# Kernel tuning notes

Hardware: AMD Instinct MI355X
Metric: run time of the kernel (lower is better)

## Reference

```python
import jax, jax.numpy as jnp
import numpy as np

EMBED_DIM = 1024
NUM_HEADS = 16
HEAD_DIM = EMBED_DIM // NUM_HEADS
B, T = 4, 2048


def setup_inputs() -> dict:
    key = jax.random.key(0)
    ks = jax.random.split(key, 10)
    s = 1.0 / np.sqrt(EMBED_DIM)
    inp = {
        "x": jax.random.normal(ks[0], (B, T, EMBED_DIM), dtype=jnp.float32),
        "mask": jnp.ones((B, T), dtype=bool),
        "q_w": jax.random.uniform(ks[1], (EMBED_DIM, EMBED_DIM), jnp.float32, -s, s),
        "q_b": jax.random.uniform(ks[2], (EMBED_DIM,), jnp.float32, -s, s),
        "k_w": jax.random.uniform(ks[3], (EMBED_DIM, EMBED_DIM), jnp.float32, -s, s),
        "k_b": jax.random.uniform(ks[4], (EMBED_DIM,), jnp.float32, -s, s),
        "v_w": jax.random.uniform(ks[5], (EMBED_DIM, EMBED_DIM), jnp.float32, -s, s),
        "v_b": jax.random.uniform(ks[6], (EMBED_DIM,), jnp.float32, -s, s),
        "o_w": jax.random.uniform(ks[7], (EMBED_DIM, EMBED_DIM), jnp.float32, -s, s),
        "o_b": jax.random.uniform(ks[8], (EMBED_DIM,), jnp.float32, -s, s),
    }
    return inp


def reference(x, mask, q_w, q_b, k_w, k_b, v_w, v_b, o_w, o_b):
    # NOTE: original module accepts `mask` but never uses it; dropout defined but never applied.
    Bn, Tn, C = x.shape
    H, D = NUM_HEADS, HEAD_DIM
    # Linear: x @ W.T + b, then split heads -> [B, H, T, D]
    Q = (x @ q_w.T + q_b).reshape(Bn, Tn, H, D).transpose(0, 2, 1, 3)
    K = (x @ k_w.T + k_b).reshape(Bn, Tn, H, D).transpose(0, 2, 1, 3)
    V = (x @ v_w.T + v_b).reshape(Bn, Tn, H, D).transpose(0, 2, 1, 3)
    scores = jnp.einsum("bhqd,bhkd->bhqk", Q, K) / jnp.sqrt(jnp.float32(D))
    attn = jax.nn.softmax(scores, axis=-1)
    out = jnp.einsum("bhqk,bhkd->bhqd", attn, V)
    out = out.transpose(0, 2, 1, 3).reshape(Bn, Tn, C)
    return out @ o_w.T + o_b
```

## Files before the change

### kernel.cpp

```cpp
#include <hip/hip_runtime.h>
#include <stdint.h>

#define B_ 4
#define T_ 2048
#define C_ 1024
#define H_ 16
#define D_ 64
#define CK 1024

typedef __attribute__((ext_vector_type(8))) short bf8;
typedef __attribute__((ext_vector_type(4))) float f4;

__device__ __forceinline__ ushort f2bf(float f) {
  union { float f; uint32_t u; } c; c.f = f;
  uint32_t u = c.u;
  uint32_t r = (u + 0x7fffu + ((u >> 16) & 1u)) >> 16;
  return (ushort)r;
}

__device__ __forceinline__ uint32_t cvtpk(float a, float b) {
  uint32_t r;
  asm("v_cvt_pk_bf16_f32 %0, %1, %2" : "=v"(r) : "v"(a), "v"(b));
  return r;
}

__global__ __launch_bounds__(256) void cast_f32_bf16(const float* __restrict__ in,
                                                     ushort* __restrict__ out, int n) {
  int i = (blockIdx.x * 256 + threadIdx.x) * 4;
  if (i >= n) return;
  float4 v = *(const float4*)(in + i);
  ushort4 o;
  o.x = f2bf(v.x); o.y = f2bf(v.y); o.z = f2bf(v.z); o.w = f2bf(v.w);
  *(ushort4*)(out + i) = o;
}

__global__ __launch_bounds__(256) void cast4_w(const float* __restrict__ w0,
                                               const float* __restrict__ w1,
                                               const float* __restrict__ w2,
                                               const float* __restrict__ w3,
                                               ushort* __restrict__ o0,
                                               ushort* __restrict__ o1,
                                               ushort* __restrict__ o2,
                                               ushort* __restrict__ o3) {
  const float* in;
  ushort* out;
  switch (blockIdx.y) {
    case 0: in = w0; out = o0; break;
    case 1: in = w1; out = o1; break;
    case 2: in = w2; out = o2; break;
    default: in = w3; out = o3; break;
  }
  int i = (blockIdx.x * 256 + threadIdx.x) * 4;
  float4 v = *(const float4*)(in + i);
  ushort4 o;
  o.x = f2bf(v.x); o.y = f2bf(v.y); o.z = f2bf(v.z); o.w = f2bf(v.w);
  *(ushort4*)(out + i) = o;
}

__global__ __launch_bounds__(256) void transpose_v(const ushort* __restrict__ in,
                                                   ushort* __restrict__ out) {
  __shared__ ushort tile[64 * 65];
  const int tid = threadIdx.x;
  const int bh = blockIdx.y, t0 = blockIdx.x * 64;
  const int r = tid >> 3, c8 = (tid & 7) * 8;

  const ushort* src = in + ((size_t)bh * T_ + t0 + r) * D_ + c8;
  *(int4*)&tile[r * 65 + c8]        = *(const int4*)&src[0];
  *(int4*)&tile[(r + 32) * 65 + c8] = *(const int4*)&src[32 * D_];
  __syncthreads();

#pragma unroll
  for (int p = 0; p < 2; ++p) {
    int d = p * 32 + (tid >> 3), tc = (tid & 7) * 8;
    ushort tmp[8];
#pragma unroll
    for (int i = 0; i < 8; ++i) tmp[i] = tile[(tc + i) * 65 + d];
    *(int4*)&out[((size_t)bh * D_ + d) * T_ + t0 + tc] = *(int4*)tmp;
  }
}

__global__ __launch_bounds__(512, 2) void gemm8(const ushort* __restrict__ A,
                                                const ushort* __restrict__ W,
                                                const float* __restrict__ b0,
                                                const float* __restrict__ b1,
                                                const float* __restrict__ b2,
                                                void* __restrict__ outp,
                                                int mode, float qsc) {
  extern __shared__ ushort smem[];
  ushort* sA = smem;
  ushort* sB = smem + 32768;

  const int tid = threadIdx.x;
  const int w = tid >> 6, l = tid & 63, lo = l & 15, hi = l >> 4;
  const int wm = w >> 2, wn = w & 3;

  const int i = blockIdx.x;
  const int m0 = ((i & 7) * 4 + ((i >> 3) & 3)) * 256;
  const int n0 = (i >> 5) * 256;

  const int rl = tid >> 3, c7 = tid & 7;
  const int scol = (c7 ^ (rl & 7)) * 8;
  const ushort* Asrc = A + (size_t)(m0 + rl) * CK + scol;
  const ushort* Bsrc = W + (size_t)(n0 + (tid >> 8) * 64 + (rl & 31)) * CK + scol;
  const int Bd0 = (tid >> 8) * 4096 + (rl & 31) * 64 + c7 * 8;

  const int sw0 = (hi ^ (lo & 7)) * 8;
  const int sw1 = ((4 + hi) ^ (lo & 7)) * 8;
  const int arow = wm * 128 + lo;
  const int brow = wn * 64 + lo;

  f4 acc[8][4];
#pragma unroll
  for (int f = 0; f < 8; ++f)
#pragma unroll
    for (int g = 0; g < 4; ++g) acc[f][g] = (f4){0.f, 0.f, 0.f, 0.f};

#define GL(src, dst) __builtin_amdgcn_global_load_lds(                                   \
      (const __attribute__((address_space(1))) void*)(src),                              \
      (__attribute__((address_space(3))) void*)(dst), 16, 0, 0)
#define STG_A(nb, mh, kn) {                                                              \
    GL(Asrc + (kn) + (size_t)((mh) * 64) * CK,       &sA[(nb)*16384 + (mh)*4096 + tid*8]);        \
    GL(Asrc + (kn) + (size_t)((mh) * 64 + 128) * CK, &sA[(nb)*16384 + 8192 + (mh)*4096 + tid*8]); }
#define STG_B(nb, nh, kn) {                                                              \
    GL(Bsrc + (kn) + (size_t)((nh) * 32) * CK,       &sB[(nb)*16384 + (nh)*2048 + Bd0]);          \
    GL(Bsrc + (kn) + (size_t)((nh) * 32 + 128) * CK, &sB[(nb)*16384 + 8192 + (nh)*2048 + Bd0]); }
#define VMC(s)  asm volatile("s_waitcnt vmcnt(" s ")" ::: "memory")
#define PH_BAR  { __builtin_amdgcn_s_barrier(); asm volatile("" ::: "memory"); }
#define LDA(cb, mh) {                                                                    \
  _Pragma("unroll")                                                                      \
  for (int f = 0; f < 4; ++f) {                                                          \
    af[f][0] = *(const bf8*)&sA[(cb)*16384 + (arow + (mh)*64 + f*16)*64 + sw0];          \
    af[f][1] = *(const bf8*)&sA[(cb)*16384 + (arow + (mh)*64 + f*16)*64 + sw1]; } }
#define LDB(cb, dst, nh) {                                                               \
  _Pragma("unroll")                                                                      \
  for (int g = 0; g < 2; ++g) {                                                          \
    dst[g][0] = *(const bf8*)&sB[(cb)*16384 + (brow + (nh)*32 + g*16)*64 + sw0];         \
    dst[g][1] = *(const bf8*)&sB[(cb)*16384 + (brow + (nh)*32 + g*16)*64 + sw1]; } }
#define MM(fo, go, bfr) {                                                                \
  __builtin_amdgcn_s_setprio(1);                                                         \
  _Pragma("unroll")                                                                      \
  for (int f = 0; f < 4; ++f)                                                            \
    _Pragma("unroll")                                                                    \
    for (int g = 0; g < 2; ++g) {                                                        \
      acc[(fo)+f][(go)+g] = __builtin_amdgcn_mfma_f32_16x16x32_bf16(af[f][0], bfr[g][0], acc[(fo)+f][(go)+g], 0, 0, 0); \
      acc[(fo)+f][(go)+g] = __builtin_amdgcn_mfma_f32_16x16x32_bf16(af[f][1], bfr[g][1], acc[(fo)+f][(go)+g], 0, 0, 0); } \
  __builtin_amdgcn_s_setprio(0); }

  bf8 af[4][2], bA[2][2], bB[2][2];

  STG_A(0, 0, 0); STG_A(0, 1, 0); STG_B(0, 0, 0); STG_B(0, 1, 0);
  VMC("0"); PH_BAR;
  int cur = 0;

  for (int t = 0; t < (CK / 64) - 1; ++t) {
    const int nb = cur ^ 1;
    const int kn = (t + 1) * 64;
    LDA(cur, 0); LDB(cur, bA, 0);
    STG_A(nb, 0, kn); STG_B(nb, 0, kn);
    VMC("6"); PH_BAR;
    MM(0, 0, bA); PH_BAR;
    LDB(cur, bB, 1);
    STG_B(nb, 1, kn);
    VMC("6"); PH_BAR;
    MM(0, 2, bB); PH_BAR;
    LDA(cur, 1);
    STG_A(nb, 1, kn);
    VMC("4"); PH_BAR;
    MM(4, 0, bA); PH_BAR;
    MM(4, 2, bB); PH_BAR;
    cur = nb;
  }
  VMC("0"); PH_BAR;
  LDA(cur, 0); LDB(cur, bA, 0); MM(0, 0, bA);
  LDB(cur, bB, 1);              MM(0, 2, bB);
  LDA(cur, 1);                  MM(4, 0, bA);
                                MM(4, 2, bB);
#undef GL
#undef STG_A
#undef STG_B
#undef VMC
#undef PH_BAR
#undef LDA
#undef LDB
#undef MM

  if (mode == 0) {
    float* O = (float*)outp;
#pragma unroll
    for (int f = 0; f < 8; ++f)
#pragma unroll
      for (int gn = 0; gn < 4; ++gn) {
        int n = n0 + wn * 64 + gn * 16 + lo;
        float bv = b0[n];
#pragma unroll
        for (int j = 0; j < 4; ++j) {
          int m = m0 + wm * 128 + f * 16 + hi * 4 + j;
          O[(size_t)m * C_ + n] = acc[f][gn][j] + bv;
        }
      }
  } else {
    const int proj = n0 >> 10;
    const float* bp = (proj == 0) ? b0 : ((proj == 1) ? b1 : b2);
    const float os = (proj == 0) ? qsc : 1.0f;
    ushort* O = (ushort*)outp + (size_t)proj * (8u << 20);
#pragma unroll
    for (int f = 0; f < 8; ++f)
#pragma unroll
      for (int gn = 0; gn < 4; ++gn) {
        int n = n0 + wn * 64 + gn * 16 + lo;
        int nl = n & 1023;
        int h = nl >> 6, d = n & 63;
        float bv = bp[nl];
#pragma unroll
        for (int j = 0; j < 4; ++j) {
          int m = m0 + wm * 128 + f * 16 + hi * 4 + j;
          int b = m >> 11, t = m & 2047;
          O[(size_t)((b << 4) + h) * (T_ * D_) + t * D_ + d] = f2bf((acc[f][gn][j] + bv) * os);
        }
      }
  }
}

__global__ __launch_bounds__(256, 4) void attn_kernel(const ushort* __restrict__ Q,
                                                      const ushort* __restrict__ Kg,
                                                      const ushort* __restrict__ VT,
                                                      ushort* __restrict__ O) {
  __shared__ ushort Ks[2][64 * 64];
  __shared__ ushort Vs[2][64 * 64];

  const int tid = threadIdx.x;
  const int w = tid >> 6, l = tid & 63, lo = l & 15, hi = l >> 4;
  const int linear = blockIdx.y * 16 + blockIdx.x;
  const int bh = (linear & 7) * 8 + ((linear >> 3) & 7);
  const int q0 = (linear >> 6) * 128 + w * 32;
  const ushort* Qb  = Q  + (size_t)bh * T_ * D_;
  const ushort* Kb  = Kg + (size_t)bh * T_ * D_;
  const ushort* VTb = VT + (size_t)bh * D_ * T_;

  bf8 qf[2][2];
#pragma unroll
  for (int qs = 0; qs < 2; ++qs)
#pragma unroll
    for (int c = 0; c < 2; ++c)
      qf[qs][c] = *(const bf8*)&Qb[(q0 + qs * 16 + lo) * D_ + c * 32 + hi * 8];

  f4 o[2][4], accL[2];
#pragma unroll
  for (int qs = 0; qs < 2; ++qs) {
    accL[qs] = (f4){0.f, 0.f, 0.f, 0.f};
#pragma unroll
    for (int dt = 0; dt < 4; ++dt) o[qs][dt] = (f4){0.f, 0.f, 0.f, 0.f};
  }
  const short ONE = 0x3F80;
  const bf8 ones = (bf8){ONE, ONE, ONE, ONE, ONE, ONE, ONE, ONE};

  const int rowA  = tid >> 3;
  const int colsw = ((tid & 7) ^ (rowA & 7)) * 8;
  const int permA = ((rowA >> 2) & 3) * 8 + ((rowA >> 4) & 1) * 4 + (rowA & 3);
  const ushort* Ksrc0 = Kb  + (size_t)permA * D_ + colsw;
  const ushort* Ksrc1 = Kb  + (size_t)(32 + permA) * D_ + colsw;
  const ushort* Vsrc0 = VTb + (size_t)rowA * T_ + colsw;
  const ushort* Vsrc1 = VTb + (size_t)(rowA + 32) * T_ + colsw;

  const int swz = (lo & 7) << 3;
  const int NT = T_ / 64;

#define STAGE(b, kvo)                                                                              \
  {                                                                                                \
    __builtin_amdgcn_global_load_lds((const __attribute__((address_space(1))) void*)(Ksrc0 + (size_t)(kvo) * D_), \
                                     (__attribute__((address_space(3))) void*)&Ks[b][tid * 8], 16, 0, 0);          \
    __builtin_amdgcn_global_load_lds((const __attribute__((address_space(1))) void*)(Ksrc1 + (size_t)(kvo) * D_), \
                                     (__attribute__((address_space(3))) void*)&Ks[b][2048 + tid * 8], 16, 0, 0);   \
    __builtin_amdgcn_global_load_lds((const __attribute__((address_space(1))) void*)(Vsrc0 + (kvo)),               \
                                     (__attribute__((address_space(3))) void*)&Vs[b][tid * 8], 16, 0, 0);          \
    __builtin_amdgcn_global_load_lds((const __attribute__((address_space(1))) void*)(Vsrc1 + (kvo)),               \
                                     (__attribute__((address_space(3))) void*)&Vs[b][2048 + tid * 8], 16, 0, 0);   \
  }

  STAGE(0, 0);
  __syncthreads();
  int cur = 0;

  for (int t = 0; t < NT; ++t) {
    if (t + 1 < NT) STAGE(cur ^ 1, (t + 1) * 64);

    const ushort* Kc = &Ks[cur][0];
    const ushort* Vc = &Vs[cur][0];

    bf8 kf[4][2], vf[4][2];
#pragma unroll
    for (int n = 0; n < 4; ++n) {
      kf[n][0] = *(const bf8*)&Kc[(n * 16 + lo) * 64 + ((hi * 8) ^ swz)];
      kf[n][1] = *(const bf8*)&Kc[(n * 16 + lo) * 64 + ((32 + hi * 8) ^ swz)];
    }
#pragma unroll
    for (int dt = 0; dt < 4; ++dt) {
      vf[dt][0] = *(const bf8*)&Vc[(dt * 16 + lo) * 64 + ((hi * 8) ^ swz)];
      vf[dt][1] = *(const bf8*)&Vc[(dt * 16 + lo) * 64 + ((32 + hi * 8) ^ swz)];
    }

#pragma unroll
    for (int qs = 0; qs < 2; ++qs) {
      f4 z[4];
#pragma unroll
      for (int n = 0; n < 4; ++n) {
        f4 zz = (f4){0.f, 0.f, 0.f, 0.f};
        zz = __builtin_amdgcn_mfma_f32_16x16x32_bf16(kf[n][0], qf[qs][0], zz, 0, 0, 0);
        zz = __builtin_amdgcn_mfma_f32_16x16x32_bf16(kf[n][1], qf[qs][1], zz, 0, 0, 0);
        z[n] = zz;
      }

      uint32_t pd[8];
#pragma unroll
      for (int n = 0; n < 4; ++n) {
        float e0 = __builtin_amdgcn_exp2f(z[n][0]);
        float e1 = __builtin_amdgcn_exp2f(z[n][1]);
        float e2 = __builtin_amdgcn_exp2f(z[n][2]);
        float e3 = __builtin_amdgcn_exp2f(z[n][3]);
        pd[n * 2 + 0] = cvtpk(e0, e1);
        pd[n * 2 + 1] = cvtpk(e2, e3);
      }
      union U8 { uint32_t u[4]; bf8 v; } u0, u1;
      u0.u[0] = pd[0]; u0.u[1] = pd[1]; u0.u[2] = pd[2]; u0.u[3] = pd[3];
      u1.u[0] = pd[4]; u1.u[1] = pd[5]; u1.u[2] = pd[6]; u1.u[3] = pd[7];

      accL[qs] = __builtin_amdgcn_mfma_f32_16x16x32_bf16(u0.v, ones, accL[qs], 0, 0, 0);
      accL[qs] = __builtin_amdgcn_mfma_f32_16x16x32_bf16(u1.v, ones, accL[qs], 0, 0, 0);

#pragma unroll
      for (int dt = 0; dt < 4; ++dt) {
        o[qs][dt] = __builtin_amdgcn_mfma_f32_16x16x32_bf16(u0.v, vf[dt][0], o[qs][dt], 0, 0, 0);
        o[qs][dt] = __builtin_amdgcn_mfma_f32_16x16x32_bf16(u1.v, vf[dt][1], o[qs][dt], 0, 0, 0);
      }
    }

    __syncthreads();
    cur ^= 1;
  }
#undef STAGE

  const int b = bh >> 4, h = bh & 15;
#pragma unroll
  for (int qs = 0; qs < 2; ++qs)
#pragma unroll
    for (int j = 0; j < 4; ++j) {
      float invL = 1.0f / accL[qs][j];
      int q = q0 + qs * 16 + hi * 4 + j;
#pragma unroll
      for (int dt = 0; dt < 4; ++dt)
        O[(size_t)(b * T_ + q) * C_ + h * D_ + dt * 16 + lo] = f2bf(o[qs][dt][j] * invL);
    }
}

extern "C" void kernel_launch(void* const* d_in, const int* in_sizes, int n_in,
                              void* d_out, int out_size, void* d_ws, size_t ws_size,
                              hipStream_t stream) {
  const float* x  = (const float*)d_in[0];
  const float* qw = (const float*)d_in[2];
  const float* qb = (const float*)d_in[3];
  const float* kw = (const float*)d_in[4];
  const float* kb = (const float*)d_in[5];
  const float* vw = (const float*)d_in[6];
  const float* vb = (const float*)d_in[7];
  const float* ow = (const float*)d_in[8];
  const float* ob = (const float*)d_in[9];
  float* out = (float*)d_out;

  char* ws = (char*)d_ws;
  ushort* xbf   = (ushort*)ws;
  ushort* VTws  = (ushort*)ws;
  ushort* qwbf  = (ushort*)(ws + (16u << 20));
  ushort* kwbf  = qwbf + (1u << 20);
  ushort* vwbf  = kwbf + (1u << 20);
  ushort* owbf  = vwbf + (1u << 20);
  ushort* Qws   = (ushort*)(ws + (24u << 20));
  ushort* Vws   = (ushort*)(ws + (56u << 20));
  ushort* attnw = (ushort*)(ws + (72u << 20));

  hipFuncSetAttribute((const void*)gemm8, hipFuncAttributeMaxDynamicSharedMemorySize, 131072);

  const int NX = B_ * T_ * C_;
  const int NW = C_ * C_;
  cast_f32_bf16<<<NX / 4 / 256, 256, 0, stream>>>(x, xbf, NX);
  cast4_w<<<dim3(NW / 4 / 256, 4), 256, 0, stream>>>(qw, kw, vw, ow, qwbf, kwbf, vwbf, owbf);

  const float QSC = 0.125f * 1.44269504f;
  gemm8<<<384, 512, 131072, stream>>>(xbf, qwbf, qb, kb, vb, Qws, 1, QSC);

  transpose_v<<<dim3(T_ / 64, B_ * H_), 256, 0, stream>>>(Vws, VTws);

  attn_kernel<<<dim3(T_ / 128, B_ * H_), 256, 0, stream>>>(Qws, Qws + (size_t)(8u << 20), VTws, attnw);

  gemm8<<<128, 512, 131072, stream>>>(attnw, owbf, ob, nullptr, nullptr, out, 0, 1.0f);
}
```

Before: 184.6 us.

## Shrink GEMM block tile to 128x256 to double grid size

Changes the GEMM tile from 256x256 to 128x256 (M halved), halving the A staging buffer and accumulator array, and doubles the number of blocks for both the QKV and output projections. The goal is better CU fill: the output projection previously launched only 128 blocks on a 256-CU device, and the smaller LDS footprint may allow more resident blocks. In exchange, arithmetic intensity per block drops, so B-tile (weight) traffic per FLOP rises and the software pipeline has fewer MFMA phases to hide loads behind.

```diff
diff --git a/kernel.cpp b/kernel.cpp
--- a/kernel.cpp
+++ b/kernel.cpp
@@ -88,93 +88,87 @@
                                                 int mode, float qsc) {
   extern __shared__ ushort smem[];
   ushort* sA = smem;
-  ushort* sB = smem + 32768;
+  ushort* sB = smem + 16384;
 
   const int tid = threadIdx.x;
   const int w = tid >> 6, l = tid & 63, lo = l & 15, hi = l >> 4;
   const int wm = w >> 2, wn = w & 3;
 
   const int i = blockIdx.x;
-  const int m0 = ((i & 7) * 4 + ((i >> 3) & 3)) * 256;
-  const int n0 = (i >> 5) * 256;
+  const int m0 = ((i & 7) * 8 + ((i >> 3) & 7)) * 128;
+  const int n0 = (i >> 6) * 256;
 
   const int rl = tid >> 3, c7 = tid & 7;
   const int scol = (c7 ^ (rl & 7)) * 8;
   const ushort* Asrc = A + (size_t)(m0 + rl) * CK + scol;
-  const ushort* Bsrc = W + (size_t)(n0 + (tid >> 8) * 64 + (rl & 31)) * CK + scol;
-  const int Bd0 = (tid >> 8) * 4096 + (rl & 31) * 64 + c7 * 8;
+  const int Brow0 = ((rl >> 5) * 64) + (rl & 31);
+  const ushort* Bsrc = W + (size_t)(n0 + Brow0) * CK + scol;
+  const int Bdst0 = Brow0 * 64 + c7 * 8;
 
   const int sw0 = (hi ^ (lo & 7)) * 8;
   const int sw1 = ((4 + hi) ^ (lo & 7)) * 8;
-  const int arow = wm * 128 + lo;
+  const int arow = wm * 64 + lo;
   const int brow = wn * 64 + lo;
 
-  f4 acc[8][4];
-#pragma unroll
-  for (int f = 0; f < 8; ++f)
+  f4 acc[4][4];
+#pragma unroll
+  for (int f = 0; f < 4; ++f)
 #pragma unroll
     for (int g = 0; g < 4; ++g) acc[f][g] = (f4){0.f, 0.f, 0.f, 0.f};
 
 #define GL(src, dst) __builtin_amdgcn_global_load_lds(                                   \
       (const __attribute__((address_space(1))) void*)(src),                              \
       (__attribute__((address_space(3))) void*)(dst), 16, 0, 0)
-#define STG_A(nb, mh, kn) {                                                              \
-    GL(Asrc + (kn) + (size_t)((mh) * 64) * CK,       &sA[(nb)*16384 + (mh)*4096 + tid*8]);        \
-    GL(Asrc + (kn) + (size_t)((mh) * 64 + 128) * CK, &sA[(nb)*16384 + 8192 + (mh)*4096 + tid*8]); }
-#define STG_B(nb, nh, kn) {                                                              \
-    GL(Bsrc + (kn) + (size_t)((nh) * 32) * CK,       &sB[(nb)*16384 + (nh)*2048 + Bd0]);          \
-    GL(Bsrc + (kn) + (size_t)((nh) * 32 + 128) * CK, &sB[(nb)*16384 + 8192 + (nh)*2048 + Bd0]); }
+#define STG_A(nb, kn) {                                                                  \
+    GL(Asrc + (kn),                    &sA[(nb)*8192 + tid*8]);                          \
+    GL(Asrc + (kn) + (size_t)64 * CK,  &sA[(nb)*8192 + 4096 + tid*8]); }
+#define STG_B(nb, h, kn) {                                                               \
+    GL(Bsrc + (kn) + (size_t)((h)*32) * CK,        &sB[(nb)*16384 + (h)*2048 + Bdst0]);           \
+    GL(Bsrc + (kn) + (size_t)((h)*32 + 128) * CK,  &sB[(nb)*16384 + (h)*2048 + 8192 + Bdst0]); }
 #define VMC(s)  asm volatile("s_waitcnt vmcnt(" s ")" ::: "memory")
 #define PH_BAR  { __builtin_amdgcn_s_barrier(); asm volatile("" ::: "memory"); }
-#define LDA(cb, mh) {                                                                    \
+#define LDA(cb) {                                                                        \
   _Pragma("unroll")                                                                      \
   for (int f = 0; f < 4; ++f) {                                                          \
-    af[f][0] = *(const bf8*)&sA[(cb)*16384 + (arow + (mh)*64 + f*16)*64 + sw0];          \
-    af[f][1] = *(const bf8*)&sA[(cb)*16384 + (arow + (mh)*64 + f*16)*64 + sw1]; } }
-#define LDB(cb, dst, nh) {                                                               \
+    af[f][0] = *(const bf8*)&sA[(cb)*8192 + (arow + f*16)*64 + sw0];                     \
+    af[f][1] = *(const bf8*)&sA[(cb)*8192 + (arow + f*16)*64 + sw1]; } }
+#define LDB(cb, dst, h) {                                                                \
   _Pragma("unroll")                                                                      \
   for (int g = 0; g < 2; ++g) {                                                          \
-    dst[g][0] = *(const bf8*)&sB[(cb)*16384 + (brow + (nh)*32 + g*16)*64 + sw0];         \
-    dst[g][1] = *(const bf8*)&sB[(cb)*16384 + (brow + (nh)*32 + g*16)*64 + sw1]; } }
-#define MM(fo, go, bfr) {                                                                \
+    dst[g][0] = *(const bf8*)&sB[(cb)*16384 + (brow + (h)*32 + g*16)*64 + sw0];          \
+    dst[g][1] = *(const bf8*)&sB[(cb)*16384 + (brow + (h)*32 + g*16)*64 + sw1]; } }
+#define MM(h, bfr) {                                                                     \
   __builtin_amdgcn_s_setprio(1);                                                         \
   _Pragma("unroll")                                                                      \
   for (int f = 0; f < 4; ++f)                                                            \
     _Pragma("unroll")                                                                    \
     for (int g = 0; g < 2; ++g) {                                                        \
-      acc[(fo)+f][(go)+g] = __builtin_amdgcn_mfma_f32_16x16x32_bf16(af[f][0], bfr[g][0], acc[(fo)+f][(go)+g], 0, 0, 0); \
-      acc[(fo)+f][(go)+g] = __builtin_amdgcn_mfma_f32_16x16x32_bf16(af[f][1], bfr[g][1], acc[(fo)+f][(go)+g], 0, 0, 0); } \
+      acc[f][(h)*2+g] = __builtin_amdgcn_mfma_f32_16x16x32_bf16(af[f][0], bfr[g][0], acc[f][(h)*2+g], 0, 0, 0); \
+      acc[f][(h)*2+g] = __builtin_amdgcn_mfma_f32_16x16x32_bf16(af[f][1], bfr[g][1], acc[f][(h)*2+g], 0, 0, 0); } \
   __builtin_amdgcn_s_setprio(0); }
 
   bf8 af[4][2], bA[2][2], bB[2][2];
 
-  STG_A(0, 0, 0); STG_A(0, 1, 0); STG_B(0, 0, 0); STG_B(0, 1, 0);
+  STG_A(0, 0); STG_B(0, 0, 0); STG_B(0, 1, 0);
   VMC("0"); PH_BAR;
   int cur = 0;
 
   for (int t = 0; t < (CK / 64) - 1; ++t) {
     const int nb = cur ^ 1;
     const int kn = (t + 1) * 64;
-    LDA(cur, 0); LDB(cur, bA, 0);
-    STG_A(nb, 0, kn); STG_B(nb, 0, kn);
+    LDA(cur); LDB(cur, bA, 0);
+    STG_A(nb, kn); STG_B(nb, 0, kn);
     VMC("6"); PH_BAR;
-    MM(0, 0, bA); PH_BAR;
+    MM(0, bA); PH_BAR;
     LDB(cur, bB, 1);
     STG_B(nb, 1, kn);
     VMC("6"); PH_BAR;
-    MM(0, 2, bB); PH_BAR;
-    LDA(cur, 1);
-    STG_A(nb, 1, kn);
-    VMC("4"); PH_BAR;
-    MM(4, 0, bA); PH_BAR;
-    MM(4, 2, bB); PH_BAR;
+    MM(1, bB); PH_BAR;
     cur = nb;
   }
   VMC("0"); PH_BAR;
-  LDA(cur, 0); LDB(cur, bA, 0); MM(0, 0, bA);
-  LDB(cur, bB, 1);              MM(0, 2, bB);
-  LDA(cur, 1);                  MM(4, 0, bA);
-                                MM(4, 2, bB);
+  LDA(cur); LDB(cur, bA, 0); MM(0, bA);
+  LDB(cur, bB, 1);           MM(1, bB);
 #undef GL
 #undef STG_A
 #undef STG_B
@@ -187,14 +181,14 @@
   if (mode == 0) {
     float* O = (float*)outp;
 #pragma unroll
-    for (int f = 0; f < 8; ++f)
+    for (int f = 0; f < 4; ++f)
 #pragma unroll
       for (int gn = 0; gn < 4; ++gn) {
         int n = n0 + wn * 64 + gn * 16 + lo;
         float bv = b0[n];
 #pragma unroll
         for (int j = 0; j < 4; ++j) {
-          int m = m0 + wm * 128 + f * 16 + hi * 4 + j;
+          int m = m0 + wm * 64 + f * 16 + hi * 4 + j;
           O[(size_t)m * C_ + n] = acc[f][gn][j] + bv;
         }
       }
@@ -204,7 +198,7 @@
     const float os = (proj == 0) ? qsc : 1.0f;
     ushort* O = (ushort*)outp + (size_t)proj * (8u << 20);
 #pragma unroll
-    for (int f = 0; f < 8; ++f)
+    for (int f = 0; f < 4; ++f)
 #pragma unroll
       for (int gn = 0; gn < 4; ++gn) {
         int n = n0 + wn * 64 + gn * 16 + lo;
@@ -213,7 +207,7 @@
         float bv = bp[nl];
 #pragma unroll
         for (int j = 0; j < 4; ++j) {
-          int m = m0 + wm * 128 + f * 16 + hi * 4 + j;
+          int m = m0 + wm * 64 + f * 16 + hi * 4 + j;
           int b = m >> 11, t = m & 2047;
           O[(size_t)((b << 4) + h) * (T_ * D_) + t * D_ + d] = f2bf((acc[f][gn][j] + bv) * os);
         }
@@ -377,7 +371,7 @@
   ushort* Vws   = (ushort*)(ws + (56u << 20));
   ushort* attnw = (ushort*)(ws + (72u << 20));
 
-  hipFuncSetAttribute((const void*)gemm8, hipFuncAttributeMaxDynamicSharedMemorySize, 131072);
+  hipFuncSetAttribute((const void*)gemm8, hipFuncAttributeMaxDynamicSharedMemorySize, 98304);
 
   const int NX = B_ * T_ * C_;
   const int NW = C_ * C_;
@@ -385,11 +379,11 @@
   cast4_w<<<dim3(NW / 4 / 256, 4), 256, 0, stream>>>(qw, kw, vw, ow, qwbf, kwbf, vwbf, owbf);
 
   const float QSC = 0.125f * 1.44269504f;
-  gemm8<<<384, 512, 131072, stream>>>(xbf, qwbf, qb, kb, vb, Qws, 1, QSC);
+  gemm8<<<768, 512, 98304, stream>>>(xbf, qwbf, qb, kb, vb, Qws, 1, QSC);
 
   transpose_v<<<dim3(T_ / 64, B_ * H_), 256, 0, stream>>>(Vws, VTws);
 
   attn_kernel<<<dim3(T_ / 128, B_ * H_), 256, 0, stream>>>(Qws, Qws + (size_t)(8u << 20), VTws, attnw);
 
-  gemm8<<<128, 512, 131072, stream>>>(attnw, owbf, ob, nullptr, nullptr, out, 0, 1.0f);
-}
+  gemm8<<<256, 512, 98304, stream>>>(attnw, owbf, ob, nullptr, nullptr, out, 0, 1.0f);
+}
```

Result: faster. 174.2 us (-5.6%).
